# Performance work log

Measured on AMD Instinct MI355X. Metric: run time of the kernel, lower is better.

Reference implementation:

```python
import jax, jax.numpy as jnp
import numpy as np

MC = 64  # mc_samples; fill=1.0 -> k == k_ball so neighbor ordering is irrelevant


def swish(x):
    return x * jax.nn.sigmoid(x)


def setup_inputs() -> dict:
    key = jax.random.key(0)
    ks = jax.random.split(key, 12)
    bs, n, g_dim = 4, 1024, 6
    c_in = c_out = 256
    H, hid = 8, 16

    def lin(k, i, o):
        return (jax.random.normal(k, (i, o), jnp.float32) / np.sqrt(i).astype(np.float32))

    return {
        "pairwise_g": jax.random.normal(ks[0], (bs, n, n, g_dim), jnp.float32),
        "coset_functions": jax.random.normal(ks[1], (bs, n, c_in), jnp.float32),
        "mask": jax.random.randint(ks[2], (bs, n), 0, 2) > 0,
        # per-head location-kernel MLP (MultiheadWeightNet: g_dim -> hid -> hid -> 1)
        "loc_W1": jax.random.normal(ks[3], (H, g_dim, hid), jnp.float32) / np.sqrt(g_dim).astype(np.float32),
        "loc_b1": jnp.zeros((H, hid), jnp.float32),
        "loc_W2": jax.random.normal(ks[4], (H, hid, hid), jnp.float32) / np.sqrt(hid).astype(np.float32),
        "loc_b2": jnp.zeros((H, hid), jnp.float32),
        "loc_W3": jax.random.normal(ks[5], (H, hid, 1), jnp.float32) / np.sqrt(hid).astype(np.float32),
        "loc_b3": jnp.zeros((H, 1), jnp.float32),
        # DotProductKernel projections
        "Wq": lin(ks[6], c_in, c_in), "bq": jnp.zeros((c_in,), jnp.float32),
        "Wk": lin(ks[7], c_in, c_in), "bk": jnp.zeros((c_in,), jnp.float32),
        # value (input_linear) and output projections
        "W_in": lin(ks[8], c_in, c_out), "b_in": jnp.zeros((c_out,), jnp.float32),
        "W_out": lin(ks[9], c_out, c_out), "b_out": jnp.zeros((c_out,), jnp.float32),
    }


def reference(pairwise_g, coset_functions, mask, loc_W1, loc_b1, loc_W2, loc_b2,
              loc_W3, loc_b3, Wq, bq, Wk, bk, W_in, b_in, W_out, b_out):
    bs, n, _, g_dim = pairwise_g.shape
    c_in = coset_functions.shape[-1]
    H = loc_W1.shape[0]
    dh = c_in // H
    b_idx = jnp.arange(bs)[:, None, None]

    # --- neighbourhood extraction: topk (smallest) group distances, masked keys pushed far away
    dists = jnp.linalg.norm(pairwise_g, axis=-1)                  # (b,n,n)
    dists = jnp.where(mask[:, None, :], dists, jnp.float32(1e8))
    _, nbhd_idx = jax.lax.top_k(-dists, MC)                       # (b,n,m) nearest MC keys
    nbhd_g = jnp.take_along_axis(pairwise_g, nbhd_idx[..., None], axis=2)  # (b,n,m,g)
    nbhd_mask = mask[b_idx, nbhd_idx]                             # (b,n,m)

    # --- location kernel: per-head MLP on gathered pairwise group elements
    h = swish(jnp.einsum('bnmg,hgk->bnmhk', nbhd_g, loc_W1) + loc_b1)
    h = swish(jnp.einsum('bnmhk,hkl->bnmhl', h, loc_W2) + loc_b2)
    loc = swish(jnp.einsum('bnmhk,hko->bnmho', h, loc_W3) + loc_b3)[..., 0]  # (b,n,m,H)

    # --- feature kernel: dot-product scores on gathered keys
    q = (coset_functions @ Wq + bq).reshape(bs, n, H, dh)
    k = (coset_functions @ Wk + bk).reshape(bs, n, H, dh)
    k_nbhd = k[b_idx, nbhd_idx]                                   # (b,n,m,H,dh)
    feat = jnp.einsum('bnhd,bnmhd->bnmh', q, k_nbhd) / np.sqrt(dh).astype(np.float32)

    # --- masked softmax over the neighbourhood dim (dim 2)
    scores = jnp.where(nbhd_mask[..., None], loc + feat, jnp.float32(-1e38))
    attn = jax.nn.softmax(scores, axis=2)                         # (b,n,m,H)

    # --- value projection + sparse attention (equivalent to the dense scatter+matmul,
    #     since topk neighbour indices are unique per query)
    v = (coset_functions @ W_in + b_in).reshape(bs, n, H, dh)
    v_nbhd = v[b_idx, nbhd_idx]                                   # (b,n,m,H,dh)
    out = jnp.einsum('bnmh,bnmhd->bnhd', attn, v_nbhd).reshape(bs, n, H * dh)
    out = out @ W_out + b_out
    return (pairwise_g, out, mask)
```

## Files before the change

kernel.cpp:

```cpp
#include <hip/hip_runtime.h>
#include <stdint.h>

#define BS 4
#define NN 1024
#define GD 6
#define CIN 256
#define NH 8
#define DH 32
#define HID 16
#define MCS 64

#define PG_ELEMS (BS*NN*NN*GD)
#define OUT_OFF  PG_ELEMS
#define MASK_OFF (PG_ELEMS + BS*NN*CIN)

typedef float vfloat4 __attribute__((ext_vector_type(4)));
typedef unsigned vuint4 __attribute__((ext_vector_type(4)));

#if __has_builtin(__builtin_amdgcn_rcpf)
__device__ __forceinline__ float fast_rcp(float x) { return __builtin_amdgcn_rcpf(x); }
#else
__device__ __forceinline__ float fast_rcp(float x) { return 1.0f / x; }
#endif
#if __has_builtin(__builtin_amdgcn_exp2f)
__device__ __forceinline__ float fast_exp2(float x) { return __builtin_amdgcn_exp2f(x); }
#else
__device__ __forceinline__ float fast_exp2(float x) { return exp2f(x); }
#endif
#define LOG2E 1.44269504088896340736f

__device__ __forceinline__ float swishf(float x) {
    return x * fast_rcp(1.0f + fast_exp2(x * -LOG2E));
}

__global__ __launch_bounds__(256) void gemm3(const float* __restrict__ X,
    const float* __restrict__ W0, const float* __restrict__ B0, float* __restrict__ D0,
    const float* __restrict__ W1, const float* __restrict__ B1, float* __restrict__ D1,
    const float* __restrict__ W2, const float* __restrict__ B2, float* __restrict__ D2)
{
    const float* W; const float* Bv; float* D;
    if (blockIdx.y == 0)      { W = W0; Bv = B0; D = D0; }
    else if (blockIdx.y == 1) { W = W1; Bv = B1; D = D1; }
    else                      { W = W2; Bv = B2; D = D2; }
    const int tid = threadIdx.x;
    const int c4  = tid & 63;
    const int rg  = tid >> 6;
    const int r0  = blockIdx.x * 16;

    __shared__ float xsT[CIN][20];
    {
        float tmp[16];
        #pragma unroll
        for (int r = 0; r < 16; ++r) tmp[r] = X[(size_t)(r0 + r)*CIN + tid];
        vfloat4* dst = (vfloat4*)&xsT[tid][0];
        #pragma unroll
        for (int j = 0; j < 4; ++j)
            dst[j] = (vfloat4){tmp[4*j+0], tmp[4*j+1], tmp[4*j+2], tmp[4*j+3]};
    }
    __syncthreads();

    vfloat4 a0 = (vfloat4){0.f,0.f,0.f,0.f};
    vfloat4 a1 = a0, a2 = a0, a3 = a0;
    const vfloat4* W4 = (const vfloat4*)W;
    #pragma unroll 4
    for (int k = 0; k < CIN; ++k) {
        vfloat4 w  = W4[(size_t)k*64 + c4];
        vfloat4 xr = *(const vfloat4*)&xsT[k][rg*4];
        a0 += xr.x * w;
        a1 += xr.y * w;
        a2 += xr.z * w;
        a3 += xr.w * w;
    }
    vfloat4 bb = ((const vfloat4*)Bv)[c4];
    vfloat4* D4 = (vfloat4*)D;
    const size_t rbase = (size_t)(r0 + rg*4);
    D4[(rbase+0)*64 + c4] = a0 + bb;
    D4[(rbase+1)*64 + c4] = a1 + bb;
    D4[(rbase+2)*64 + c4] = a2 + bb;
    D4[(rbase+3)*64 + c4] = a3 + bb;
}

__global__ __launch_bounds__(256, 8) void attn_topk(
    const float* __restrict__ pg, const int* __restrict__ mask,
    const float* __restrict__ lW1g, const float* __restrict__ lb1g,
    const float* __restrict__ lW2g, const float* __restrict__ lb2g,
    const float* __restrict__ lW3g, const float* __restrict__ lb3g,
    const float* __restrict__ Q, const float* __restrict__ Kc, const float* __restrict__ Vc,
    float* __restrict__ O, float* __restrict__ pg_out, float* __restrict__ mask_out)
{
    const int i = blockIdx.x, b = blockIdx.y, tid = threadIdx.x;
    const int lane = tid & 63;

    __shared__ __align__(16) unsigned selbuf[512];
    __shared__ float sg[MCS*7];
    __shared__ int nj[MCS];
    __shared__ __align__(16) unsigned joff[MCS];
    __shared__ vfloat4 obuf[4][64];
    __shared__ unsigned wsum[4];
    __shared__ unsigned sel_bin, sel_need, s_cnt, s_eqcnt;

    float (*sc)[NH]   = (float (*)[NH])selbuf;
    unsigned* hist    = selbuf;
    unsigned* eqlist  = selbuf + 256;

    const int* mrow = mask + b*NN;
    if (tid == 0) mask_out[b*NN + i] = mrow[i] ? 1.0f : 0.0f;

    const size_t rowoff = (size_t)(b*NN + i) * (NN*GD);
    const vfloat4* src4 = (const vfloat4*)(pg + rowoff);
    vfloat4* dst4 = (vfloat4*)(pg_out + rowoff);
    #pragma unroll
    for (int t = 0; t < 6; ++t) {
        vfloat4 v = src4[tid + 256*t];
        __builtin_nontemporal_store(v, &dst4[tid + 256*t]);
    }
    vfloat4 q4 = ((const vfloat4*)Q)[(size_t)(b*NN + i)*64 + (tid & 63)];

    const int4 mv = ((const int4*)mrow)[tid];
    const vfloat4* gg = src4 + tid*6;
    vfloat4 g0 = gg[0], g1 = gg[1], g2 = gg[2], g3 = gg[3], g4 = gg[4], g5 = gg[5];
    float rv[4][6];
    rv[0][0]=g0.x; rv[0][1]=g0.y; rv[0][2]=g0.z; rv[0][3]=g0.w; rv[0][4]=g1.x; rv[0][5]=g1.y;
    rv[1][0]=g1.z; rv[1][1]=g1.w; rv[1][2]=g2.x; rv[1][3]=g2.y; rv[1][4]=g2.z; rv[1][5]=g2.w;
    rv[2][0]=g3.x; rv[2][1]=g3.y; rv[2][2]=g3.z; rv[2][3]=g3.w; rv[2][4]=g4.x; rv[2][5]=g4.y;
    rv[3][0]=g4.z; rv[3][1]=g4.w; rv[3][2]=g5.x; rv[3][3]=g5.y; rv[3][4]=g5.z; rv[3][5]=g5.w;
    const int vb[4] = { mv.x, mv.y, mv.z, mv.w };
    unsigned key[4];
    #pragma unroll
    for (int r = 0; r < 4; ++r) {
        float d2 = rv[r][0]*rv[r][0] + rv[r][1]*rv[r][1] + rv[r][2]*rv[r][2]
                 + rv[r][3]*rv[r][3] + rv[r][4]*rv[r][4] + rv[r][5]*rv[r][5];
        key[r] = __float_as_uint(vb[r] ? d2 : 1e30f);
    }

    unsigned prefix = 0;
    int need = MCS;
    for (int level = 0; level < 4; ++level) {
        const int shift = 24 - 8*level;
        hist[tid] = 0;
        __syncthreads();
        if (level == 0) {
            #pragma unroll
            for (int r = 0; r < 4; ++r) {
                unsigned d = key[r] >> 24;
                unsigned long long todo = __ballot(true);
                while (todo) {
                    int leader = (int)(__ffsll((unsigned long long)todo) - 1);
                    unsigned dl = __shfl(d, leader);
                    unsigned long long match = __ballot(d == dl);
                    if (lane == leader) atomicAdd(&hist[dl], (unsigned)__popcll(match));
                    todo &= ~match;
                }
            }
        } else {
            const unsigned pmask = 0xFFFFFFFFu << (shift + 8);
            #pragma unroll
            for (int r = 0; r < 4; ++r)
                if ((key[r] & pmask) == prefix)
                    atomicAdd(&hist[(key[r] >> shift) & 0xFFu], 1u);
        }
        __syncthreads();
        unsigned own = hist[tid];
        unsigned v = own;
        #pragma unroll
        for (int off = 1; off < 64; off <<= 1) {
            unsigned nv = __shfl_up(v, off);
            if (lane >= off) v += nv;
        }
        if (lane == 63) wsum[tid >> 6] = v;
        __syncthreads();
        unsigned basec = 0;
        for (int w = 0; w < (tid >> 6); ++w) basec += wsum[w];
        unsigned incl = v + basec;
        unsigned excl = incl - own;
        if (excl < (unsigned)need && (unsigned)need <= incl) {
            sel_bin = (unsigned)tid;
            sel_need = (unsigned)need - excl;
        }
        __syncthreads();
        prefix |= (sel_bin << shift);
        need = (int)sel_need;
    }
    const unsigned T = prefix;
    const int needT = need;

    if (tid == 0) { s_cnt = 0; s_eqcnt = 0; }
    __syncthreads();
    #pragma unroll
    for (int r = 0; r < 4; ++r) {
        unsigned kk = key[r];
        int j = tid*4 + r;
        if (kk < T) {
            unsigned p = atomicAdd(&s_cnt, 1u);
            nj[p] = j | (vb[r] ? 0 : (int)0x80000000);
            #pragma unroll
            for (int g = 0; g < GD; ++g) sg[p*7 + g] = rv[r][g];
        } else if (kk == T) {
            unsigned e = atomicAdd(&s_eqcnt, 1u);
            if (e < 64) eqlist[e] = (unsigned)j;
        }
    }
    __syncthreads();
    const int cbase = (int)s_cnt;
    if (tid == 0) {
        int ec = (int)s_eqcnt; if (ec > 64) ec = 64;
        for (int s2 = 0; s2 < needT; ++s2) {
            int bi = -1, bj = 0x7FFFFFFF;
            for (int e = 0; e < ec; ++e) {
                int jj = (int)eqlist[e];
                if (jj < bj) { bj = jj; bi = e; }
            }
            if (bi >= 0) {
                eqlist[bi] = 0x7FFFFFFFu;
                nj[cbase + s2] = bj | (mrow[bj] ? 0 : (int)0x80000000);
            }
        }
    }
    __syncthreads();
    #pragma unroll
    for (int r = 0; r < 4; ++r) {
        if (key[r] == T) {
            int j = tid*4 + r;
            for (int s2 = 0; s2 < needT; ++s2)
                if ((nj[cbase + s2] & 0x7FFFFFFF) == j) {
                    #pragma unroll
                    for (int g = 0; g < GD; ++g) sg[(cbase + s2)*7 + g] = rv[r][g];
                }
        }
    }
    __syncthreads();

    if (tid < MCS) joff[tid] = ((unsigned)(b*NN + (nj[tid] & 0x7FFFFFFF))) << 6;

    #pragma unroll
    for (int pass = 0; pass < 2; ++pass) {
        const int h = __builtin_amdgcn_readfirstlane((tid >> 6) + pass*4);
        const int m = lane;
        const float* W1h = lW1g + h*(GD*HID);
        const float* B1h = lb1g + h*HID;
        const float* W2h = lW2g + h*(HID*HID);
        const float* B2h = lb2g + h*HID;
        const float* W3h = lW3g + h*HID;
        float gv[GD];
        #pragma unroll
        for (int g = 0; g < GD; ++g) gv[g] = sg[m*7 + g];
        float h1[HID];
        #pragma unroll
        for (int kk = 0; kk < HID; ++kk) {
            float a = B1h[kk];
            #pragma unroll
            for (int g = 0; g < GD; ++g) a += gv[g] * W1h[g*HID + kk];
            h1[kk] = swishf(a);
        }
        float h2[HID];
        #pragma unroll
        for (int l = 0; l < HID; ++l) {
            float a = B2h[l];
            #pragma unroll
            for (int kk = 0; kk < HID; ++kk) a += h1[kk] * W2h[kk*HID + l];
            h2[l] = swishf(a);
        }
        float a3 = lb3g[h];
        #pragma unroll
        for (int kk = 0; kk < HID; ++kk) a3 += h2[kk] * W3h[kk];
        sc[m][h] = (nj[m] < 0) ? -1e38f : swishf(a3);
    }
    __syncthreads();

    const int q = tid & 63;
    const int p = tid >> 6;
    const int hh = q >> 3;
    q4 *= 0.17677669529663688f;
    const vfloat4* Kc4 = (const vfloat4*)Kc;
    const vuint4* jo4 = (const vuint4*)(joff + (p << 4));
    #pragma unroll
    for (int mg = 0; mg < 4; ++mg) {
        vuint4 o4 = jo4[mg];
        #pragma unroll
        for (int r = 0; r < 4; ++r) {
            const int mm = (p << 4) + (mg << 2) + r;
            vfloat4 kv = Kc4[o4[r] + (unsigned)q];
            float d = q4.x * kv.x;
            d = fmaf(q4.y, kv.y, d);
            d = fmaf(q4.z, kv.z, d);
            d = fmaf(q4.w, kv.w, d);
            d += __shfl_xor(d, 1);
            d += __shfl_xor(d, 2);
            d += __shfl_xor(d, 4);
            if ((q & 7) == 0) sc[mm][hh] += d;
        }
    }
    __syncthreads();

    #pragma unroll
    for (int pass = 0; pass < 2; ++pass) {
        int h = (tid >> 6) + pass*4;
        float s = sc[lane][h];
        float mx = s;
        #pragma unroll
        for (int off = 32; off; off >>= 1) mx = fmaxf(mx, __shfl_xor(mx, off));
        float e = fast_exp2((s - mx) * LOG2E);
        float sum = e;
        #pragma unroll
        for (int off = 32; off; off >>= 1) sum += __shfl_xor(sum, off);
        sc[lane][h] = e * fast_rcp(sum);
    }
    __syncthreads();

    {
        const vfloat4* Vc4 = (const vfloat4*)Vc;
        vfloat4 acc = (vfloat4){0.f,0.f,0.f,0.f};
        #pragma unroll
        for (int mg = 0; mg < 4; ++mg) {
            vuint4 o4 = jo4[mg];
            #pragma unroll
            for (int r = 0; r < 4; ++r) {
                const int mm = (p << 4) + (mg << 2) + r;
                float a = sc[mm][hh];
                vfloat4 v4 = Vc4[o4[r] + (unsigned)q];
                acc += a * v4;
            }
        }
        obuf[p][q] = acc;
    }
    __syncthreads();
    {
        const float* ob = (const float*)obuf;
        float s = ob[tid] + ob[256 + tid] + ob[512 + tid] + ob[768 + tid];
        O[(size_t)(b*NN + i)*CIN + tid] = s;
    }
}

extern "C" void kernel_launch(void* const* d_in, const int* in_sizes, int n_in,
                              void* d_out, int out_size, void* d_ws, size_t ws_size,
                              hipStream_t stream) {
    const float* pg   = (const float*)d_in[0];
    const float* x    = (const float*)d_in[1];
    const int*   mask = (const int*)d_in[2];
    const float* lW1  = (const float*)d_in[3];
    const float* lb1  = (const float*)d_in[4];
    const float* lW2  = (const float*)d_in[5];
    const float* lb2  = (const float*)d_in[6];
    const float* lW3  = (const float*)d_in[7];
    const float* lb3  = (const float*)d_in[8];
    const float* Wq   = (const float*)d_in[9];
    const float* bq   = (const float*)d_in[10];
    const float* Wk   = (const float*)d_in[11];
    const float* bk   = (const float*)d_in[12];
    const float* Wv   = (const float*)d_in[13];
    const float* bv   = (const float*)d_in[14];
    const float* Wo   = (const float*)d_in[15];
    const float* bo   = (const float*)d_in[16];

    float* out = (float*)d_out;
    float* Q  = (float*)d_ws;
    float* Kc = Q  + (size_t)BS*NN*CIN;
    float* Vc = Kc + (size_t)BS*NN*CIN;
    float* O  = Vc + (size_t)BS*NN*CIN;

    gemm3<<<dim3(BS*NN/16, 3), 256, 0, stream>>>(x, Wq, bq, Q, Wk, bk, Kc, Wv, bv, Vc);
    attn_topk<<<dim3(NN, BS), 256, 0, stream>>>(pg, mask, lW1, lb1, lW2, lb2, lW3, lb3,
                                                Q, Kc, Vc, O, out, out + MASK_OFF);
    gemm3<<<dim3(BS*NN/16, 1), 256, 0, stream>>>(O, Wo, bo, out + OUT_OFF,
                                                 Wo, bo, out + OUT_OFF,
                                                 Wo, bo, out + OUT_OFF);
}
```

Measured before the change: 338.8 us.

## Reuse coalesced pg loads for distance via LDS atomics and defer copy stores

The attention kernel no longer loads each pairwise_g row twice, once coalesced for the copy and once strided for distances. It computes squared distances from the coalesced copy registers, accumulating partial sums into shared memory with atomics, then gathers the 64 selected neighbour g-vectors straight from global memory. The non-temporal copy stores are moved after selection, and the MLP phase gets a raised wave priority. The output GEMM is templated to 8 rows per block to double its grid, at the cost of extra LDS atomics and holding 24 copy registers live across the selection phase.

New measurement: 356.9 us. 5.3% more time.

```diff
diff --git a/kernel.cpp b/kernel.cpp
--- a/kernel.cpp
+++ b/kernel.cpp
@@ -15,6 +15,7 @@
 #define MASK_OFF (PG_ELEMS + BS*NN*CIN)
 
 typedef float vfloat4 __attribute__((ext_vector_type(4)));
+typedef float vfloat2 __attribute__((ext_vector_type(2)));
 typedef unsigned vuint4 __attribute__((ext_vector_type(4)));
 
 #if __has_builtin(__builtin_amdgcn_rcpf)
@@ -33,6 +34,7 @@
     return x * fast_rcp(1.0f + fast_exp2(x * -LOG2E));
 }
 
+template<int RPB>
 __global__ __launch_bounds__(256) void gemm3(const float* __restrict__ X,
     const float* __restrict__ W0, const float* __restrict__ B0, float* __restrict__ D0,
     const float* __restrict__ W1, const float* __restrict__ B1, float* __restrict__ D1,
@@ -45,39 +47,44 @@
     const int tid = threadIdx.x;
     const int c4  = tid & 63;
     const int rg  = tid >> 6;
-    const int r0  = blockIdx.x * 16;
-
-    __shared__ float xsT[CIN][20];
+    const int r0  = blockIdx.x * RPB;
+    constexpr int RG = RPB / 4;
+
+    __shared__ float xsT[CIN][RPB + 4];
     {
-        float tmp[16];
-        #pragma unroll
-        for (int r = 0; r < 16; ++r) tmp[r] = X[(size_t)(r0 + r)*CIN + tid];
-        vfloat4* dst = (vfloat4*)&xsT[tid][0];
-        #pragma unroll
-        for (int j = 0; j < 4; ++j)
-            dst[j] = (vfloat4){tmp[4*j+0], tmp[4*j+1], tmp[4*j+2], tmp[4*j+3]};
-    }
-    __syncthreads();
-
-    vfloat4 a0 = (vfloat4){0.f,0.f,0.f,0.f};
-    vfloat4 a1 = a0, a2 = a0, a3 = a0;
+        float tmp[RPB];
+        #pragma unroll
+        for (int r = 0; r < RPB; ++r) tmp[r] = X[(size_t)(r0 + r)*CIN + tid];
+        #pragma unroll
+        for (int j = 0; j < RPB/4; ++j)
+            *(vfloat4*)&xsT[tid][4*j] = (vfloat4){tmp[4*j+0], tmp[4*j+1], tmp[4*j+2], tmp[4*j+3]};
+    }
+    __syncthreads();
+
+    vfloat4 acc[RG];
+    #pragma unroll
+    for (int r = 0; r < RG; ++r) acc[r] = (vfloat4){0.f,0.f,0.f,0.f};
     const vfloat4* W4 = (const vfloat4*)W;
     #pragma unroll 4
     for (int k = 0; k < CIN; ++k) {
-        vfloat4 w  = W4[(size_t)k*64 + c4];
-        vfloat4 xr = *(const vfloat4*)&xsT[k][rg*4];
-        a0 += xr.x * w;
-        a1 += xr.y * w;
-        a2 += xr.z * w;
-        a3 += xr.w * w;
+        vfloat4 w = W4[(size_t)k*64 + c4];
+        if constexpr (RG == 4) {
+            vfloat4 xr = *(const vfloat4*)&xsT[k][rg*4];
+            acc[0] += xr.x * w;
+            acc[1] += xr.y * w;
+            acc[2] += xr.z * w;
+            acc[3] += xr.w * w;
+        } else {
+            vfloat2 xr = *(const vfloat2*)&xsT[k][rg*2];
+            acc[0] += xr.x * w;
+            acc[1] += xr.y * w;
+        }
     }
     vfloat4 bb = ((const vfloat4*)Bv)[c4];
     vfloat4* D4 = (vfloat4*)D;
-    const size_t rbase = (size_t)(r0 + rg*4);
-    D4[(rbase+0)*64 + c4] = a0 + bb;
-    D4[(rbase+1)*64 + c4] = a1 + bb;
-    D4[(rbase+2)*64 + c4] = a2 + bb;
-    D4[(rbase+3)*64 + c4] = a3 + bb;
+    const size_t rbase = (size_t)(r0 + rg*RG);
+    #pragma unroll
+    for (int r = 0; r < RG; ++r) D4[(rbase + r)*64 + c4] = acc[r] + bb;
 }
 
 __global__ __launch_bounds__(256, 8) void attn_topk(
@@ -95,7 +102,7 @@
     __shared__ float sg[MCS*7];
     __shared__ int nj[MCS];
     __shared__ __align__(16) unsigned joff[MCS];
-    __shared__ vfloat4 obuf[4][64];
+    __shared__ __align__(16) float scratch[1024];
     __shared__ unsigned wsum[4];
     __shared__ unsigned sel_bin, sel_need, s_cnt, s_eqcnt;
 
@@ -109,28 +116,39 @@
     const size_t rowoff = (size_t)(b*NN + i) * (NN*GD);
     const vfloat4* src4 = (const vfloat4*)(pg + rowoff);
     vfloat4* dst4 = (vfloat4*)(pg_out + rowoff);
-    #pragma unroll
-    for (int t = 0; t < 6; ++t) {
-        vfloat4 v = src4[tid + 256*t];
-        __builtin_nontemporal_store(v, &dst4[tid + 256*t]);
-    }
+    vfloat4 c0 = src4[tid      ], c1 = src4[tid +  256], c2 = src4[tid +  512],
+            c3 = src4[tid + 768], c4 = src4[tid + 1024], c5 = src4[tid + 1280];
     vfloat4 q4 = ((const vfloat4*)Q)[(size_t)(b*NN + i)*64 + (tid & 63)];
-
     const int4 mv = ((const int4*)mrow)[tid];
-    const vfloat4* gg = src4 + tid*6;
-    vfloat4 g0 = gg[0], g1 = gg[1], g2 = gg[2], g3 = gg[3], g4 = gg[4], g5 = gg[5];
-    float rv[4][6];
-    rv[0][0]=g0.x; rv[0][1]=g0.y; rv[0][2]=g0.z; rv[0][3]=g0.w; rv[0][4]=g1.x; rv[0][5]=g1.y;
-    rv[1][0]=g1.z; rv[1][1]=g1.w; rv[1][2]=g2.x; rv[1][3]=g2.y; rv[1][4]=g2.z; rv[1][5]=g2.w;
-    rv[2][0]=g3.x; rv[2][1]=g3.y; rv[2][2]=g3.z; rv[2][3]=g3.w; rv[2][4]=g4.x; rv[2][5]=g4.y;
-    rv[3][0]=g4.z; rv[3][1]=g4.w; rv[3][2]=g5.x; rv[3][3]=g5.y; rv[3][4]=g5.z; rv[3][5]=g5.w;
+
+    *(vfloat4*)&scratch[tid*4] = (vfloat4){0.f,0.f,0.f,0.f};
+    __syncthreads();
+
+    const int tm3 = tid % 3;
+    #define ACC_D2(v, t) do { \
+        int p = tid + 256*(t); \
+        int pm = tm3 + ((t) % 3); if (pm >= 3) pm -= 3; \
+        int r0 = 2 * (int)(((unsigned)(p - pm)) * 0xAAAAAAABu);  \
+        vfloat4 sq = (v)*(v); \
+        float slo = sq.x + sq.y, shi = sq.z + sq.w; \
+        bool split = (pm == 1); \
+        int ra = r0 + ((pm == 2) ? 1 : 0); \
+        atomicAdd(&scratch[ra], split ? slo : (slo + shi)); \
+        if (split) atomicAdd(&scratch[r0 + 1], shi); \
+    } while (0)
+    ACC_D2(c0, 0); ACC_D2(c1, 1); ACC_D2(c2, 2);
+    ACC_D2(c3, 3); ACC_D2(c4, 4); ACC_D2(c5, 5);
+    #undef ACC_D2
+    __syncthreads();
+
     const int vb[4] = { mv.x, mv.y, mv.z, mv.w };
     unsigned key[4];
-    #pragma unroll
-    for (int r = 0; r < 4; ++r) {
-        float d2 = rv[r][0]*rv[r][0] + rv[r][1]*rv[r][1] + rv[r][2]*rv[r][2]
-                 + rv[r][3]*rv[r][3] + rv[r][4]*rv[r][4] + rv[r][5]*rv[r][5];
-        key[r] = __float_as_uint(vb[r] ? d2 : 1e30f);
+    {
+        vfloat4 dd = *(const vfloat4*)&scratch[tid*4];
+        float dv[4] = { dd.x, dd.y, dd.z, dd.w };
+        #pragma unroll
+        for (int r = 0; r < 4; ++r)
+            key[r] = __float_as_uint(vb[r] ? dv[r] : 1e30f);
     }
 
     unsigned prefix = 0;
@@ -193,8 +211,6 @@
         if (kk < T) {
             unsigned p = atomicAdd(&s_cnt, 1u);
             nj[p] = j | (vb[r] ? 0 : (int)0x80000000);
-            #pragma unroll
-            for (int g = 0; g < GD; ++g) sg[p*7 + g] = rv[r][g];
         } else if (kk == T) {
             unsigned e = atomicAdd(&s_eqcnt, 1u);
             if (e < 64) eqlist[e] = (unsigned)j;
@@ -217,21 +233,27 @@
         }
     }
     __syncthreads();
-    #pragma unroll
-    for (int r = 0; r < 4; ++r) {
-        if (key[r] == T) {
-            int j = tid*4 + r;
-            for (int s2 = 0; s2 < needT; ++s2)
-                if ((nj[cbase + s2] & 0x7FFFFFFF) == j) {
-                    #pragma unroll
-                    for (int g = 0; g < GD; ++g) sg[(cbase + s2)*7 + g] = rv[r][g];
-                }
-        }
-    }
-    __syncthreads();
-
-    if (tid < MCS) joff[tid] = ((unsigned)(b*NN + (nj[tid] & 0x7FFFFFFF))) << 6;
-
+    if (tid < MCS) {
+        int jm = nj[tid] & 0x7FFFFFFF;
+        joff[tid] = ((unsigned)(b*NN + jm)) << 6;
+        const float* gp = pg + rowoff + (size_t)jm * 6;
+        vfloat2 g01 = *(const vfloat2*)gp;
+        vfloat2 g23 = *(const vfloat2*)(gp + 2);
+        vfloat2 g45 = *(const vfloat2*)(gp + 4);
+        float* sgp = sg + tid*7;
+        sgp[0] = g01.x; sgp[1] = g01.y; sgp[2] = g23.x;
+        sgp[3] = g23.y; sgp[4] = g45.x; sgp[5] = g45.y;
+    }
+    __syncthreads();
+
+    __builtin_nontemporal_store(c0, &dst4[tid      ]);
+    __builtin_nontemporal_store(c1, &dst4[tid +  256]);
+    __builtin_nontemporal_store(c2, &dst4[tid +  512]);
+    __builtin_nontemporal_store(c3, &dst4[tid +  768]);
+    __builtin_nontemporal_store(c4, &dst4[tid + 1024]);
+    __builtin_nontemporal_store(c5, &dst4[tid + 1280]);
+
+    __builtin_amdgcn_s_setprio(1);
     #pragma unroll
     for (int pass = 0; pass < 2; ++pass) {
         const int h = __builtin_amdgcn_readfirstlane((tid >> 6) + pass*4);
@@ -321,11 +343,12 @@
                 acc += a * v4;
             }
         }
-        obuf[p][q] = acc;
+        __builtin_amdgcn_s_setprio(0);
+        ((vfloat4*)scratch)[p*64 + q] = acc;
     }
     __syncthreads();
     {
-        const float* ob = (const float*)obuf;
+        const float* ob = scratch;
         float s = ob[tid] + ob[256 + tid] + ob[512 + tid] + ob[768 + tid];
         O[(size_t)(b*NN + i)*CIN + tid] = s;
     }
@@ -358,10 +381,10 @@
     float* Vc = Kc + (size_t)BS*NN*CIN;
     float* O  = Vc + (size_t)BS*NN*CIN;
 
-    gemm3<<<dim3(BS*NN/16, 3), 256, 0, stream>>>(x, Wq, bq, Q, Wk, bk, Kc, Wv, bv, Vc);
+    gemm3<16><<<dim3(BS*NN/16, 3), 256, 0, stream>>>(x, Wq, bq, Q, Wk, bk, Kc, Wv, bv, Vc);
     attn_topk<<<dim3(NN, BS), 256, 0, stream>>>(pg, mask, lW1, lb1, lW2, lb2, lW3, lb3,
                                                 Q, Kc, Vc, O, out, out + MASK_OFF);
-    gemm3<<<dim3(BS*NN/16, 1), 256, 0, stream>>>(O, Wo, bo, out + OUT_OFF,
-                                                 Wo, bo, out + OUT_OFF,
-                                                 Wo, bo, out + OUT_OFF);
+    gemm3<8><<<dim3(BS*NN/8, 1), 256, 0, stream>>>(O, Wo, bo, out + OUT_OFF,
+                                                   Wo, bo, out + OUT_OFF,
+                                                   Wo, bo, out + OUT_OFF);
 }
```

## Overlap feature dot-products and pg copy with location MLP; double-buffer histograms

Applied to the files above, without the earlier changes.

Moves the gathered-key dot-product computation ahead of the location-kernel MLP, holding results in registers and adding them to scores later. The pairwise_g passthrough copy is deferred until after those loads so it overlaps other work, and wave priority is raised around the compute phases. Histogram levels alternate between two shared buffers, which removes one barrier per radix level and the separate counter-init barrier. The output GEMM now uses 8 rows per block to launch more blocks. The gain depends on latency hiding, at the cost of higher register pressure.

After: 359.5 us. 6.1% more time.

```diff
diff --git a/kernel.cpp b/kernel.cpp
--- a/kernel.cpp
+++ b/kernel.cpp
@@ -15,6 +15,7 @@
 #define MASK_OFF (PG_ELEMS + BS*NN*CIN)
 
 typedef float vfloat4 __attribute__((ext_vector_type(4)));
+typedef float vfloat2 __attribute__((ext_vector_type(2)));
 typedef unsigned vuint4 __attribute__((ext_vector_type(4)));
 
 #if __has_builtin(__builtin_amdgcn_rcpf)
@@ -33,6 +34,7 @@
     return x * fast_rcp(1.0f + fast_exp2(x * -LOG2E));
 }
 
+template<int RPB>
 __global__ __launch_bounds__(256) void gemm3(const float* __restrict__ X,
     const float* __restrict__ W0, const float* __restrict__ B0, float* __restrict__ D0,
     const float* __restrict__ W1, const float* __restrict__ B1, float* __restrict__ D1,
@@ -45,39 +47,44 @@
     const int tid = threadIdx.x;
     const int c4  = tid & 63;
     const int rg  = tid >> 6;
-    const int r0  = blockIdx.x * 16;
-
-    __shared__ float xsT[CIN][20];
-    {
-        float tmp[16];
-        #pragma unroll
-        for (int r = 0; r < 16; ++r) tmp[r] = X[(size_t)(r0 + r)*CIN + tid];
-        vfloat4* dst = (vfloat4*)&xsT[tid][0];
-        #pragma unroll
-        for (int j = 0; j < 4; ++j)
-            dst[j] = (vfloat4){tmp[4*j+0], tmp[4*j+1], tmp[4*j+2], tmp[4*j+3]};
-    }
-    __syncthreads();
-
-    vfloat4 a0 = (vfloat4){0.f,0.f,0.f,0.f};
-    vfloat4 a1 = a0, a2 = a0, a3 = a0;
+    const int r0  = blockIdx.x * RPB;
+    constexpr int RG = RPB / 4;
+
+    __shared__ float xsT[CIN][RPB + 4];
+    {
+        float tmp[RPB];
+        #pragma unroll
+        for (int r = 0; r < RPB; ++r) tmp[r] = X[(size_t)(r0 + r)*CIN + tid];
+        #pragma unroll
+        for (int j = 0; j < RPB/4; ++j)
+            *(vfloat4*)&xsT[tid][4*j] = (vfloat4){tmp[4*j+0], tmp[4*j+1], tmp[4*j+2], tmp[4*j+3]};
+    }
+    __syncthreads();
+
+    vfloat4 acc[RG];
+    #pragma unroll
+    for (int r = 0; r < RG; ++r) acc[r] = (vfloat4){0.f,0.f,0.f,0.f};
     const vfloat4* W4 = (const vfloat4*)W;
     #pragma unroll 4
     for (int k = 0; k < CIN; ++k) {
-        vfloat4 w  = W4[(size_t)k*64 + c4];
-        vfloat4 xr = *(const vfloat4*)&xsT[k][rg*4];
-        a0 += xr.x * w;
-        a1 += xr.y * w;
-        a2 += xr.z * w;
-        a3 += xr.w * w;
+        vfloat4 w = W4[(size_t)k*64 + c4];
+        if constexpr (RG == 4) {
+            vfloat4 xr = *(const vfloat4*)&xsT[k][rg*4];
+            acc[0] += xr.x * w;
+            acc[1] += xr.y * w;
+            acc[2] += xr.z * w;
+            acc[3] += xr.w * w;
+        } else {
+            vfloat2 xr = *(const vfloat2*)&xsT[k][rg*2];
+            acc[0] += xr.x * w;
+            acc[1] += xr.y * w;
+        }
     }
     vfloat4 bb = ((const vfloat4*)Bv)[c4];
     vfloat4* D4 = (vfloat4*)D;
-    const size_t rbase = (size_t)(r0 + rg*4);
-    D4[(rbase+0)*64 + c4] = a0 + bb;
-    D4[(rbase+1)*64 + c4] = a1 + bb;
-    D4[(rbase+2)*64 + c4] = a2 + bb;
-    D4[(rbase+3)*64 + c4] = a3 + bb;
+    const size_t rbase = (size_t)(r0 + rg*RG);
+    #pragma unroll
+    for (int r = 0; r < RG; ++r) D4[(rbase + r)*64 + c4] = acc[r] + bb;
 }
 
 __global__ __launch_bounds__(256, 8) void attn_topk(
@@ -100,23 +107,18 @@
     __shared__ unsigned sel_bin, sel_need, s_cnt, s_eqcnt;
 
     float (*sc)[NH]   = (float (*)[NH])selbuf;
-    unsigned* hist    = selbuf;
     unsigned* eqlist  = selbuf + 256;
 
     const int* mrow = mask + b*NN;
-    if (tid == 0) mask_out[b*NN + i] = mrow[i] ? 1.0f : 0.0f;
+    if (tid == 0) { mask_out[b*NN + i] = mrow[i] ? 1.0f : 0.0f; s_cnt = 0; s_eqcnt = 0; }
 
     const size_t rowoff = (size_t)(b*NN + i) * (NN*GD);
     const vfloat4* src4 = (const vfloat4*)(pg + rowoff);
     vfloat4* dst4 = (vfloat4*)(pg_out + rowoff);
-    #pragma unroll
-    for (int t = 0; t < 6; ++t) {
-        vfloat4 v = src4[tid + 256*t];
-        __builtin_nontemporal_store(v, &dst4[tid + 256*t]);
-    }
+
     vfloat4 q4 = ((const vfloat4*)Q)[(size_t)(b*NN + i)*64 + (tid & 63)];
-
     const int4 mv = ((const int4*)mrow)[tid];
+
     const vfloat4* gg = src4 + tid*6;
     vfloat4 g0 = gg[0], g1 = gg[1], g2 = gg[2], g3 = gg[3], g4 = gg[4], g5 = gg[5];
     float rv[4][6];
@@ -133,12 +135,15 @@
         key[r] = __float_as_uint(vb[r] ? d2 : 1e30f);
     }
 
+    selbuf[tid] = 0;
+    selbuf[tid + 256] = 0;
+    __syncthreads();
+
     unsigned prefix = 0;
     int need = MCS;
     for (int level = 0; level < 4; ++level) {
         const int shift = 24 - 8*level;
-        hist[tid] = 0;
-        __syncthreads();
+        unsigned* hist = selbuf + ((level & 1) << 8);
         if (level == 0) {
             #pragma unroll
             for (int r = 0; r < 4; ++r) {
@@ -161,6 +166,7 @@
         }
         __syncthreads();
         unsigned own = hist[tid];
+        hist[tid] = 0;
         unsigned v = own;
         #pragma unroll
         for (int off = 1; off < 64; off <<= 1) {
@@ -184,8 +190,6 @@
     const unsigned T = prefix;
     const int needT = need;
 
-    if (tid == 0) { s_cnt = 0; s_eqcnt = 0; }
-    __syncthreads();
     #pragma unroll
     for (int r = 0; r < 4; ++r) {
         unsigned kk = key[r];
@@ -228,10 +232,47 @@
                 }
         }
     }
-    __syncthreads();
-
     if (tid < MCS) joff[tid] = ((unsigned)(b*NN + (nj[tid] & 0x7FFFFFFF))) << 6;
-
+    __syncthreads();
+
+    const int q = tid & 63;
+    const int p = tid >> 6;
+    const int hh = q >> 3;
+    q4 *= 0.17677669529663688f;
+    const vfloat4* Kc4 = (const vfloat4*)Kc;
+    float pack0 = 0.f, pack1 = 0.f;
+    {
+        const vuint4* jo4 = (const vuint4*)(joff + (p << 4));
+        vuint4 oa = jo4[0], ob = jo4[1], oc = jo4[2], od = jo4[3];
+        #define FEAT_ONE(OFF, RR, PACK) do { \
+            vfloat4 kv = Kc4[(OFF) + (unsigned)q]; \
+            float d = q4.x * kv.x; \
+            d = fmaf(q4.y, kv.y, d); \
+            d = fmaf(q4.z, kv.z, d); \
+            d = fmaf(q4.w, kv.w, d); \
+            d += __shfl_xor(d, 1); \
+            d += __shfl_xor(d, 2); \
+            d += __shfl_xor(d, 4); \
+            if ((q & 7) == (RR)) (PACK) = d; \
+        } while (0)
+        FEAT_ONE(oa.x, 0, pack0); FEAT_ONE(oa.y, 1, pack0);
+        FEAT_ONE(oa.z, 2, pack0); FEAT_ONE(oa.w, 3, pack0);
+        FEAT_ONE(ob.x, 4, pack0); FEAT_ONE(ob.y, 5, pack0);
+        FEAT_ONE(ob.z, 6, pack0); FEAT_ONE(ob.w, 7, pack0);
+        FEAT_ONE(oc.x, 0, pack1); FEAT_ONE(oc.y, 1, pack1);
+        FEAT_ONE(oc.z, 2, pack1); FEAT_ONE(oc.w, 3, pack1);
+        FEAT_ONE(od.x, 4, pack1); FEAT_ONE(od.y, 5, pack1);
+        FEAT_ONE(od.z, 6, pack1); FEAT_ONE(od.w, 7, pack1);
+        #undef FEAT_ONE
+    }
+
+    #pragma unroll
+    for (int t = 0; t < 6; ++t) {
+        vfloat4 v = src4[tid + 256*t];
+        __builtin_nontemporal_store(v, &dst4[tid + 256*t]);
+    }
+
+    __builtin_amdgcn_s_setprio(1);
     #pragma unroll
     for (int pass = 0; pass < 2; ++pass) {
         const int h = __builtin_amdgcn_readfirstlane((tid >> 6) + pass*4);
@@ -267,28 +308,11 @@
     }
     __syncthreads();
 
-    const int q = tid & 63;
-    const int p = tid >> 6;
-    const int hh = q >> 3;
-    q4 *= 0.17677669529663688f;
-    const vfloat4* Kc4 = (const vfloat4*)Kc;
-    const vuint4* jo4 = (const vuint4*)(joff + (p << 4));
-    #pragma unroll
-    for (int mg = 0; mg < 4; ++mg) {
-        vuint4 o4 = jo4[mg];
-        #pragma unroll
-        for (int r = 0; r < 4; ++r) {
-            const int mm = (p << 4) + (mg << 2) + r;
-            vfloat4 kv = Kc4[o4[r] + (unsigned)q];
-            float d = q4.x * kv.x;
-            d = fmaf(q4.y, kv.y, d);
-            d = fmaf(q4.z, kv.z, d);
-            d = fmaf(q4.w, kv.w, d);
-            d += __shfl_xor(d, 1);
-            d += __shfl_xor(d, 2);
-            d += __shfl_xor(d, 4);
-            if ((q & 7) == 0) sc[mm][hh] += d;
-        }
+    {
+        float* scf = (float*)selbuf;
+        const int a0 = p*128 + ((q & 7) << 3) + (q >> 3);
+        scf[a0]      += pack0;
+        scf[a0 + 64] += pack1;
     }
     __syncthreads();
 
@@ -309,18 +333,21 @@
 
     {
         const vfloat4* Vc4 = (const vfloat4*)Vc;
+        const vuint4* jo4 = (const vuint4*)(joff + (p << 4));
+        vuint4 oa = jo4[0], ob = jo4[1], oc = jo4[2], od = jo4[3];
         vfloat4 acc = (vfloat4){0.f,0.f,0.f,0.f};
-        #pragma unroll
-        for (int mg = 0; mg < 4; ++mg) {
-            vuint4 o4 = jo4[mg];
-            #pragma unroll
-            for (int r = 0; r < 4; ++r) {
-                const int mm = (p << 4) + (mg << 2) + r;
-                float a = sc[mm][hh];
-                vfloat4 v4 = Vc4[o4[r] + (unsigned)q];
-                acc += a * v4;
-            }
-        }
+        #define OUT_ONE(OFF, MM) do { \
+            float a = sc[MM][hh]; \
+            vfloat4 v4 = Vc4[(OFF) + (unsigned)q]; \
+            acc += a * v4; \
+        } while (0)
+        const int mb = p << 4;
+        OUT_ONE(oa.x, mb+0);  OUT_ONE(oa.y, mb+1);  OUT_ONE(oa.z, mb+2);  OUT_ONE(oa.w, mb+3);
+        OUT_ONE(ob.x, mb+4);  OUT_ONE(ob.y, mb+5);  OUT_ONE(ob.z, mb+6);  OUT_ONE(ob.w, mb+7);
+        OUT_ONE(oc.x, mb+8);  OUT_ONE(oc.y, mb+9);  OUT_ONE(oc.z, mb+10); OUT_ONE(oc.w, mb+11);
+        OUT_ONE(od.x, mb+12); OUT_ONE(od.y, mb+13); OUT_ONE(od.z, mb+14); OUT_ONE(od.w, mb+15);
+        #undef OUT_ONE
+        __builtin_amdgcn_s_setprio(0);
         obuf[p][q] = acc;
     }
     __syncthreads();
@@ -358,10 +385,10 @@
     float* Vc = Kc + (size_t)BS*NN*CIN;
     float* O  = Vc + (size_t)BS*NN*CIN;
 
-    gemm3<<<dim3(BS*NN/16, 3), 256, 0, stream>>>(x, Wq, bq, Q, Wk, bk, Kc, Wv, bv, Vc);
+    gemm3<16><<<dim3(BS*NN/16, 3), 256, 0, stream>>>(x, Wq, bq, Q, Wk, bk, Kc, Wv, bv, Vc);
     attn_topk<<<dim3(NN, BS), 256, 0, stream>>>(pg, mask, lW1, lb1, lW2, lb2, lW3, lb3,
                                                 Q, Kc, Vc, O, out, out + MASK_OFF);
-    gemm3<<<dim3(BS*NN/16, 1), 256, 0, stream>>>(O, Wo, bo, out + OUT_OFF,
-                                                 Wo, bo, out + OUT_OFF,
-                                                 Wo, bo, out + OUT_OFF);
+    gemm3<8><<<dim3(BS*NN/8, 1), 256, 0, stream>>>(O, Wo, bo, out + OUT_OFF,
+                                                   Wo, bo, out + OUT_OFF,
+                                                   Wo, bo, out + OUT_OFF);
 }
```
